# Performance work log

Hardware: AMD Instinct MI355X
Metric: run time of the kernel (lower is better)

Reference implementation:

```python
import jax, jax.numpy as jnp
import numpy as np

N = 8192       # num_nodes
E = 262144     # num_edges (avg degree 32)
D_IN = 256
D_H = 256
D_OUT = 256
BN_EPS = 1e-5


def _linear_params(key, din, dout):
    # torch nn.Linear default init: U(-1/sqrt(din), 1/sqrt(din))
    s = 1.0 / np.sqrt(din)
    kw, kb = jax.random.split(key)
    W = jax.random.uniform(kw, (dout, din), jnp.float32, -s, s)
    b = jax.random.uniform(kb, (dout,), jnp.float32, -s, s)
    return W, b


def setup_inputs() -> dict:
    key = jax.random.key(0)
    ks = jax.random.split(key, 6)
    x = jax.random.normal(ks[0], (N, D_IN), jnp.float32)
    edge_index = jax.random.randint(ks[1], (2, E), 0, N, dtype=jnp.int64)
    W1, b1 = _linear_params(ks[2], D_IN, D_H)
    W2, b2 = _linear_params(ks[3], D_H, D_H)
    W3, b3 = _linear_params(ks[4], D_H, D_OUT)
    return {
        "x": x, "edge_index": edge_index,
        "W1": W1, "b1": b1, "W2": W2, "b2": b2, "W3": W3, "b3": b3,
        "g1": jnp.ones((D_H,), jnp.float32), "be1": jnp.zeros((D_H,), jnp.float32),
        "g2": jnp.ones((D_H,), jnp.float32), "be2": jnp.zeros((D_H,), jnp.float32),
        "g3": jnp.ones((D_OUT,), jnp.float32), "be3": jnp.zeros((D_OUT,), jnp.float32),
    }


def _build_norm(edge_index):
    # add self loops, scatter 1.0 into dense NxN adjacency (duplicates collapse via set)
    loop = jnp.arange(N, dtype=edge_index.dtype)
    rows = jnp.concatenate([edge_index[0], loop])
    cols = jnp.concatenate([edge_index[1], loop])
    adj = jnp.zeros((N, N), jnp.float32).at[rows, cols].set(1.0)
    deg = adj.sum(axis=1)
    dinv = jnp.where(deg > 0, deg ** -0.5, 0.0)  # inf -> 0 as in original
    return dinv[:, None] * adj * dinv[None, :]


def _gcn(x, norm, W, b):
    # linear then symmetric-normalized aggregation
    return norm @ (x @ W.T + b)


def _bn(x, g, b):
    # BatchNorm1d with batch statistics (biased var), eps=1e-5
    mu = x.mean(axis=0)
    var = x.var(axis=0)
    return (x - mu) * jax.lax.rsqrt(var + BN_EPS) * g + b


def reference(x, edge_index, W1, b1, W2, b2, W3, b3, g1, be1, g2, be2, g3, be3):
    norm = _build_norm(edge_index)
    h = jax.nn.relu(_bn(_gcn(x, norm, W1, b1), g1, be1))
    h = jax.nn.relu(_bn(_gcn(h, norm, W2, b2), g2, be2))
    h = _bn(_gcn(h, norm, W3, b3), g3, be3)
    return h
```

## Files before the change

kernel.cpp:

```cpp
#include <hip/hip_runtime.h>

#define N_NODES 8192
#define N_EDGES 262144
#define D 256
#define ADJ_WORDS 256
#define MAX_DEG 128
#define AGG_BLOCKS 2048
#define RED_BLOCKS 128

typedef __attribute__((ext_vector_type(8))) short bf16x8;
typedef __attribute__((ext_vector_type(4))) float f32x4;

__device__ __forceinline__ short f2bf(float f) {
    unsigned u = __builtin_bit_cast(unsigned, f);
    u += 0x7fffu + ((u >> 16) & 1);
    return (short)(u >> 16);
}
__device__ __forceinline__ float bf2f(unsigned short u) {
    return __builtin_bit_cast(float, ((unsigned)u) << 16);
}

__global__ void build_adj(const int* __restrict__ ei, unsigned* __restrict__ adj,
                          int* __restrict__ deg) {
    int i = blockIdx.x * blockDim.x + threadIdx.x;
    int r, c;
    if (i < N_EDGES) {
        r = ei[i];
        c = ei[N_EDGES + i];
    } else if (i < N_EDGES + N_NODES) {
        r = i - N_EDGES;
        c = r;
    } else {
        return;
    }
    unsigned bit = 1u << (c & 31);
    unsigned old = atomicOr(&adj[r * ADJ_WORDS + (c >> 5)], bit);
    if (!(old & bit)) atomicAdd(&deg[r], 1);
}

__global__ __launch_bounds__(256) void build_nbrs(const unsigned* __restrict__ adj,
                                                  const int* __restrict__ deg,
                                                  int* __restrict__ nbr_idx,
                                                  float* __restrict__ nbr_w,
                                                  const float* __restrict__ W1,
                                                  const float* __restrict__ W2,
                                                  const float* __restrict__ W3,
                                                  unsigned short* __restrict__ Wb1,
                                                  unsigned short* __restrict__ Wb2,
                                                  unsigned short* __restrict__ Wb3) {
    if (blockIdx.x >= N_NODES) {
        int i = (blockIdx.x - N_NODES) * 256 + threadIdx.x;
        int which = i >> 16, j = i & 65535;
        const float* src = which == 0 ? W1 : which == 1 ? W2 : W3;
        unsigned short* dst = which == 0 ? Wb1 : which == 1 ? Wb2 : Wb3;
        dst[j] = (unsigned short)f2bf(src[j]);
        return;
    }
    const int r = blockIdx.x;
    const int t = threadIdx.x;
    const int lane = t & 63, wave = t >> 6;
    unsigned m = adj[r * ADJ_WORDS + t];
    int cnt = __popc(m);
    int x = cnt;
    #pragma unroll
    for (int off = 1; off < 64; off <<= 1) {
        int v = __shfl_up(x, off, 64);
        if (lane >= off) x += v;
    }
    __shared__ int wtot[4];
    if (lane == 63) wtot[wave] = x;
    __syncthreads();
    int woff = 0;
    #pragma unroll
    for (int w = 0; w < 4; w++) woff += (w < wave) ? wtot[w] : 0;
    int base = woff + x - cnt;
    const float dr = rsqrtf((float)deg[r]);
    int* oi = nbr_idx + (size_t)r * MAX_DEG;
    float* ow = nbr_w + (size_t)r * MAX_DEG;
    while (m) {
        int b = __ffs(m) - 1;
        m &= m - 1;
        int c = (t << 5) + b;
        if (base < MAX_DEG) {
            oi[base] = c;
            ow[base] = dr * rsqrtf((float)deg[c]);
        }
        base++;
    }
}

template <bool APPLY, bool RELU>
__global__ __launch_bounds__(256) void gemm_mfma(const float* __restrict__ Xsrc,
                                                 const float* __restrict__ psum2,
                                                 const float* __restrict__ psq2,
                                                 const float* __restrict__ g,
                                                 const float* __restrict__ be,
                                                 const unsigned short* __restrict__ Wb,
                                                 const float* __restrict__ bias,
                                                 unsigned short* __restrict__ Hb) {
    __shared__ float ssc[256], ssh[256];
    const int tid = threadIdx.x;
    if (APPLY) {
        float s = 0.f, q = 0.f;
        #pragma unroll 8
        for (int i = 0; i < RED_BLOCKS; i++) {
            s += psum2[i * 256 + tid];
            q += psq2[i * 256 + tid];
        }
        float mu = s * (1.0f / N_NODES);
        float var = q * (1.0f / N_NODES) - mu * mu;
        float rstd = rsqrtf(var + 1e-5f);
        float sc = g[tid] * rstd;
        ssc[tid] = sc;
        ssh[tid] = be[tid] - mu * sc;
        __syncthreads();
    }

    const int bn = blockIdx.x * 64;
    const int bm = blockIdx.y * 128;
    const int wave = tid >> 6, lane = tid & 63;
    const int l16 = lane & 15, q = lane >> 4;
    const int mrow0 = bm + wave * 32;

    f32x4 acc[2][4];
    #pragma unroll
    for (int i = 0; i < 2; i++)
        #pragma unroll
        for (int j = 0; j < 4; j++) acc[i][j] = (f32x4){0.f, 0.f, 0.f, 0.f};

    for (int k0 = 0; k0 < D; k0 += 32) {
        const int kq = k0 + q * 8;
        bf16x8 xb[2];
        float4 sc0, sc1, sh0, sh1;
        if (APPLY) {
            sc0 = *(const float4*)(ssc + kq);
            sc1 = *(const float4*)(ssc + kq + 4);
            sh0 = *(const float4*)(ssh + kq);
            sh1 = *(const float4*)(ssh + kq + 4);
        }
        #pragma unroll
        for (int mf = 0; mf < 2; mf++) {
            const float* xr = Xsrc + (size_t)(mrow0 + mf * 16 + l16) * D + kq;
            float4 a = *(const float4*)xr;
            float4 b = *(const float4*)(xr + 4);
            float v[8] = {a.x, a.y, a.z, a.w, b.x, b.y, b.z, b.w};
            if (APPLY) {
                float sc[8] = {sc0.x, sc0.y, sc0.z, sc0.w, sc1.x, sc1.y, sc1.z, sc1.w};
                float sh[8] = {sh0.x, sh0.y, sh0.z, sh0.w, sh1.x, sh1.y, sh1.z, sh1.w};
                #pragma unroll
                for (int j = 0; j < 8; j++) {
                    v[j] = fmaf(v[j], sc[j], sh[j]);
                    if (RELU) v[j] = fmaxf(v[j], 0.0f);
                }
            }
            #pragma unroll
            for (int j = 0; j < 8; j++) xb[mf][j] = f2bf(v[j]);
        }
        #pragma unroll
        for (int nf = 0; nf < 4; nf++) {
            bf16x8 wa = *(const bf16x8*)(Wb + (size_t)(bn + nf * 16 + l16) * D + kq);
            #pragma unroll
            for (int mf = 0; mf < 2; mf++)
                acc[mf][nf] = __builtin_amdgcn_mfma_f32_16x16x32_bf16(wa, xb[mf], acc[mf][nf], 0, 0, 0);
        }
    }

    #pragma unroll
    for (int mf = 0; mf < 2; mf++) {
        const int m = mrow0 + mf * 16 + l16;
        #pragma unroll
        for (int nf = 0; nf < 4; nf++) {
            const int nb = bn + nf * 16 + q * 4;
            float4 b4 = *(const float4*)(bias + nb);
            short4 o;
            o.x = f2bf(acc[mf][nf][0] + b4.x);
            o.y = f2bf(acc[mf][nf][1] + b4.y);
            o.z = f2bf(acc[mf][nf][2] + b4.z);
            o.w = f2bf(acc[mf][nf][3] + b4.w);
            *(short4*)(Hb + (size_t)m * D + nb) = o;
        }
    }
}

__global__ __launch_bounds__(256) void aggregate_bf16(const int* __restrict__ nbr_idx,
                                                      const float* __restrict__ nbr_w,
                                                      const int* __restrict__ deg,
                                                      const unsigned short* __restrict__ Hb,
                                                      float* __restrict__ G,
                                                      float* __restrict__ psum,
                                                      float* __restrict__ psumsq) {
    const int wave = threadIdx.x >> 6;
    const int lane = threadIdx.x & 63;
    const int ch = lane * 4;
    const int r = blockIdx.x * 4 + wave;

    int dg = deg[r]; if (dg > MAX_DEG) dg = MAX_DEG;
    const int* idx = nbr_idx + (size_t)r * MAX_DEG;
    const float* wt = nbr_w + (size_t)r * MAX_DEG;
    float4 A = make_float4(0.f, 0.f, 0.f, 0.f);
    int j = 0;
    for (; j + 8 <= dg; j += 8) {
        int4 c0 = *(const int4*)(idx + j);
        int4 c1 = *(const int4*)(idx + j + 4);
        float4 w0 = *(const float4*)(wt + j);
        float4 w1 = *(const float4*)(wt + j + 4);
        ushort4 u0 = *(const ushort4*)(Hb + (size_t)c0.x * D + ch);
        ushort4 u1 = *(const ushort4*)(Hb + (size_t)c0.y * D + ch);
        ushort4 u2 = *(const ushort4*)(Hb + (size_t)c0.z * D + ch);
        ushort4 u3 = *(const ushort4*)(Hb + (size_t)c0.w * D + ch);
        ushort4 u4 = *(const ushort4*)(Hb + (size_t)c1.x * D + ch);
        ushort4 u5 = *(const ushort4*)(Hb + (size_t)c1.y * D + ch);
        ushort4 u6 = *(const ushort4*)(Hb + (size_t)c1.z * D + ch);
        ushort4 u7 = *(const ushort4*)(Hb + (size_t)c1.w * D + ch);
        A.x = fmaf(w0.x, bf2f(u0.x), A.x); A.y = fmaf(w0.x, bf2f(u0.y), A.y);
        A.z = fmaf(w0.x, bf2f(u0.z), A.z); A.w = fmaf(w0.x, bf2f(u0.w), A.w);
        A.x = fmaf(w0.y, bf2f(u1.x), A.x); A.y = fmaf(w0.y, bf2f(u1.y), A.y);
        A.z = fmaf(w0.y, bf2f(u1.z), A.z); A.w = fmaf(w0.y, bf2f(u1.w), A.w);
        A.x = fmaf(w0.z, bf2f(u2.x), A.x); A.y = fmaf(w0.z, bf2f(u2.y), A.y);
        A.z = fmaf(w0.z, bf2f(u2.z), A.z); A.w = fmaf(w0.z, bf2f(u2.w), A.w);
        A.x = fmaf(w0.w, bf2f(u3.x), A.x); A.y = fmaf(w0.w, bf2f(u3.y), A.y);
        A.z = fmaf(w0.w, bf2f(u3.z), A.z); A.w = fmaf(w0.w, bf2f(u3.w), A.w);
        A.x = fmaf(w1.x, bf2f(u4.x), A.x); A.y = fmaf(w1.x, bf2f(u4.y), A.y);
        A.z = fmaf(w1.x, bf2f(u4.z), A.z); A.w = fmaf(w1.x, bf2f(u4.w), A.w);
        A.x = fmaf(w1.y, bf2f(u5.x), A.x); A.y = fmaf(w1.y, bf2f(u5.y), A.y);
        A.z = fmaf(w1.y, bf2f(u5.z), A.z); A.w = fmaf(w1.y, bf2f(u5.w), A.w);
        A.x = fmaf(w1.z, bf2f(u6.x), A.x); A.y = fmaf(w1.z, bf2f(u6.y), A.y);
        A.z = fmaf(w1.z, bf2f(u6.z), A.z); A.w = fmaf(w1.z, bf2f(u6.w), A.w);
        A.x = fmaf(w1.w, bf2f(u7.x), A.x); A.y = fmaf(w1.w, bf2f(u7.y), A.y);
        A.z = fmaf(w1.w, bf2f(u7.z), A.z); A.w = fmaf(w1.w, bf2f(u7.w), A.w);
    }
    for (; j + 4 <= dg; j += 4) {
        int4 c0 = *(const int4*)(idx + j);
        float4 w0 = *(const float4*)(wt + j);
        ushort4 u0 = *(const ushort4*)(Hb + (size_t)c0.x * D + ch);
        ushort4 u1 = *(const ushort4*)(Hb + (size_t)c0.y * D + ch);
        ushort4 u2 = *(const ushort4*)(Hb + (size_t)c0.z * D + ch);
        ushort4 u3 = *(const ushort4*)(Hb + (size_t)c0.w * D + ch);
        A.x = fmaf(w0.x, bf2f(u0.x), A.x); A.y = fmaf(w0.x, bf2f(u0.y), A.y);
        A.z = fmaf(w0.x, bf2f(u0.z), A.z); A.w = fmaf(w0.x, bf2f(u0.w), A.w);
        A.x = fmaf(w0.y, bf2f(u1.x), A.x); A.y = fmaf(w0.y, bf2f(u1.y), A.y);
        A.z = fmaf(w0.y, bf2f(u1.z), A.z); A.w = fmaf(w0.y, bf2f(u1.w), A.w);
        A.x = fmaf(w0.z, bf2f(u2.x), A.x); A.y = fmaf(w0.z, bf2f(u2.y), A.y);
        A.z = fmaf(w0.z, bf2f(u2.z), A.z); A.w = fmaf(w0.z, bf2f(u2.w), A.w);
        A.x = fmaf(w0.w, bf2f(u3.x), A.x); A.y = fmaf(w0.w, bf2f(u3.y), A.y);
        A.z = fmaf(w0.w, bf2f(u3.z), A.z); A.w = fmaf(w0.w, bf2f(u3.w), A.w);
    }
    for (; j < dg; j++) {
        int c = idx[j];
        float w = wt[j];
        ushort4 u = *(const ushort4*)(Hb + (size_t)c * D + ch);
        A.x = fmaf(w, bf2f(u.x), A.x); A.y = fmaf(w, bf2f(u.y), A.y);
        A.z = fmaf(w, bf2f(u.z), A.z); A.w = fmaf(w, bf2f(u.w), A.w);
    }
    *(float4*)(G + (size_t)r * D + ch) = A;

    __shared__ float ls[4][256], lss[4][256];
    ls[wave][ch] = A.x; ls[wave][ch + 1] = A.y; ls[wave][ch + 2] = A.z; ls[wave][ch + 3] = A.w;
    lss[wave][ch] = A.x * A.x; lss[wave][ch + 1] = A.y * A.y;
    lss[wave][ch + 2] = A.z * A.z; lss[wave][ch + 3] = A.w * A.w;
    __syncthreads();
    const int t = threadIdx.x;
    psum[blockIdx.x * 256 + t] = ls[0][t] + ls[1][t] + ls[2][t] + ls[3][t];
    psumsq[blockIdx.x * 256 + t] = lss[0][t] + lss[1][t] + lss[2][t] + lss[3][t];
}

__global__ __launch_bounds__(256) void reduce_partials(const float* __restrict__ psum,
                                                       const float* __restrict__ psumsq,
                                                       float* __restrict__ psum2,
                                                       float* __restrict__ psumsq2) {
    const int b = blockIdx.x;
    const int t = threadIdx.x;
    const int rows = AGG_BLOCKS / RED_BLOCKS;
    float s = 0.0f, q = 0.0f;
    #pragma unroll
    for (int i = 0; i < rows; i++) {
        s += psum[(size_t)(b * rows + i) * 256 + t];
        q += psumsq[(size_t)(b * rows + i) * 256 + t];
    }
    psum2[b * 256 + t] = s;
    psumsq2[b * 256 + t] = q;
}

__global__ __launch_bounds__(256) void bn_apply_out(const float* __restrict__ G,
                                                    const float* __restrict__ psum2,
                                                    const float* __restrict__ psq2,
                                                    const float* __restrict__ g,
                                                    const float* __restrict__ be,
                                                    float* __restrict__ Out) {
    __shared__ float ssc[256], ssh[256];
    const int tid = threadIdx.x;
    {
        float s = 0.f, q = 0.f;
        #pragma unroll 8
        for (int i = 0; i < RED_BLOCKS; i++) {
            s += psum2[i * 256 + tid];
            q += psq2[i * 256 + tid];
        }
        float mu = s * (1.0f / N_NODES);
        float var = q * (1.0f / N_NODES) - mu * mu;
        float rstd = rsqrtf(var + 1e-5f);
        float sc = g[tid] * rstd;
        ssc[tid] = sc;
        ssh[tid] = be[tid] - mu * sc;
        __syncthreads();
    }
    const int rows_per_block = 64;
    const int r0 = blockIdx.x * rows_per_block;
    const int ch = (tid & 63) * 4;
    const int rsub = tid >> 6;
    float4 sc = *(const float4*)(ssc + ch);
    float4 sh = *(const float4*)(ssh + ch);
    for (int rr = rsub; rr < rows_per_block; rr += 4) {
        const size_t off = (size_t)(r0 + rr) * D + ch;
        float4 v = *(const float4*)(G + off);
        v.x = fmaf(v.x, sc.x, sh.x);
        v.y = fmaf(v.y, sc.y, sh.y);
        v.z = fmaf(v.z, sc.z, sh.z);
        v.w = fmaf(v.w, sc.w, sh.w);
        *(float4*)(Out + off) = v;
    }
}

extern "C" void kernel_launch(void* const* d_in, const int* in_sizes, int n_in,
                              void* d_out, int out_size, void* d_ws, size_t ws_size,
                              hipStream_t stream) {
    const float* x  = (const float*)d_in[0];
    const int*   ei = (const int*)d_in[1];
    const float* W1 = (const float*)d_in[2];
    const float* b1 = (const float*)d_in[3];
    const float* W2 = (const float*)d_in[4];
    const float* b2 = (const float*)d_in[5];
    const float* W3 = (const float*)d_in[6];
    const float* b3 = (const float*)d_in[7];
    const float* g1 = (const float*)d_in[8];
    const float* be1 = (const float*)d_in[9];
    const float* g2 = (const float*)d_in[10];
    const float* be2 = (const float*)d_in[11];
    const float* g3 = (const float*)d_in[12];
    const float* be3 = (const float*)d_in[13];

    char* ws = (char*)d_ws;
    unsigned*       adj  = (unsigned*)ws;
    unsigned short* Hb   = (unsigned short*)ws;
    int*            deg  = (int*)(ws + (8 << 20));
    float*          psum2= (float*)(ws + (8 << 20) + (64 << 10));
    float*          psq2 = (float*)(ws + (8 << 20) + (192 << 10));
    unsigned short* Wb1  = (unsigned short*)(ws + (8 << 20) + (320 << 10));
    unsigned short* Wb2  = (unsigned short*)(ws + (8 << 20) + (448 << 10));
    unsigned short* Wb3  = (unsigned short*)(ws + (8 << 20) + (576 << 10));
    float*          psum = (float*)(ws + (9 << 20));
    float*          psq  = (float*)(ws + (11 << 20));
    int*            nbr_idx = (int*)  (ws + (13 << 20));
    float*          nbr_w   = (float*)(ws + (17 << 20));
    float*          G       = (float*)(ws + (21 << 20));

    hipMemsetAsync(ws, 0, (8 << 20) + (32 << 10), stream);

    build_adj<<<(N_EDGES + N_NODES + 255) / 256, 256, 0, stream>>>(ei, adj, deg);
    build_nbrs<<<N_NODES + 768, 256, 0, stream>>>(adj, deg, nbr_idx, nbr_w,
                                                  W1, W2, W3, Wb1, Wb2, Wb3);

    dim3 ggrid(D / 64, N_NODES / 128);

    gemm_mfma<false, false><<<ggrid, 256, 0, stream>>>(x, nullptr, nullptr, nullptr, nullptr,
                                                       Wb1, b1, Hb);
    aggregate_bf16<<<AGG_BLOCKS, 256, 0, stream>>>(nbr_idx, nbr_w, deg, Hb, G, psum, psq);
    reduce_partials<<<RED_BLOCKS, 256, 0, stream>>>(psum, psq, psum2, psq2);

    gemm_mfma<true, true><<<ggrid, 256, 0, stream>>>(G, psum2, psq2, g1, be1, Wb2, b2, Hb);
    aggregate_bf16<<<AGG_BLOCKS, 256, 0, stream>>>(nbr_idx, nbr_w, deg, Hb, G, psum, psq);
    reduce_partials<<<RED_BLOCKS, 256, 0, stream>>>(psum, psq, psum2, psq2);

    gemm_mfma<true, true><<<ggrid, 256, 0, stream>>>(G, psum2, psq2, g2, be2, Wb3, b3, Hb);
    aggregate_bf16<<<AGG_BLOCKS, 256, 0, stream>>>(nbr_idx, nbr_w, deg, Hb, G, psum, psq);
    reduce_partials<<<RED_BLOCKS, 256, 0, stream>>>(psum, psq, psum2, psq2);

    bn_apply_out<<<N_NODES / 64, 256, 0, stream>>>(G, psum2, psq2, g3, be3, (float*)d_out);
}
```

Baseline: 237.3 us.

## Store intermediate aggregates as bf16, shrink GEMM tile, unroll gather by 16

The first two layers' aggregation outputs are now written as bf16 instead of fp32. The following GEMM reads them as bf16, which halves the intermediate traffic between the aggregate and GEMM kernels. The GEMM M-tile is halved to 64 rows per block with one 16-row fragment per wave, doubling the block count. The aggregation gather loop is unrolled to 16 neighbours to keep more loads in flight. The bf16 rounding happens before batch-norm, which adds quantization error, and each block now reuses fewer weights.

New measurement: 251.9 us. 1.06x slower.

```diff
diff --git a/kernel.cpp b/kernel.cpp
--- a/kernel.cpp
+++ b/kernel.cpp
@@ -89,8 +89,8 @@
     }
 }
 
-template <bool APPLY, bool RELU>
-__global__ __launch_bounds__(256) void gemm_mfma(const float* __restrict__ Xsrc,
+template <bool APPLY, bool RELU, bool XBF16>
+__global__ __launch_bounds__(256) void gemm_mfma(const void* __restrict__ Xsrc,
                                                  const float* __restrict__ psum2,
                                                  const float* __restrict__ psq2,
                                                  const float* __restrict__ g,
@@ -117,75 +117,72 @@
     }
 
     const int bn = blockIdx.x * 64;
-    const int bm = blockIdx.y * 128;
+    const int bm = blockIdx.y * 64;
     const int wave = tid >> 6, lane = tid & 63;
     const int l16 = lane & 15, q = lane >> 4;
-    const int mrow0 = bm + wave * 32;
-
-    f32x4 acc[2][4];
+    const int mrow = bm + wave * 16 + l16;
+
+    f32x4 acc[4];
     #pragma unroll
-    for (int i = 0; i < 2; i++)
-        #pragma unroll
-        for (int j = 0; j < 4; j++) acc[i][j] = (f32x4){0.f, 0.f, 0.f, 0.f};
+    for (int j = 0; j < 4; j++) acc[j] = (f32x4){0.f, 0.f, 0.f, 0.f};
 
     for (int k0 = 0; k0 < D; k0 += 32) {
         const int kq = k0 + q * 8;
-        bf16x8 xb[2];
-        float4 sc0, sc1, sh0, sh1;
-        if (APPLY) {
-            sc0 = *(const float4*)(ssc + kq);
-            sc1 = *(const float4*)(ssc + kq + 4);
-            sh0 = *(const float4*)(ssh + kq);
-            sh1 = *(const float4*)(ssh + kq + 4);
-        }
-        #pragma unroll
-        for (int mf = 0; mf < 2; mf++) {
-            const float* xr = Xsrc + (size_t)(mrow0 + mf * 16 + l16) * D + kq;
+        bf16x8 xb;
+        float v[8];
+        if (XBF16) {
+            bf16x8 xr = *(const bf16x8*)((const unsigned short*)Xsrc + (size_t)mrow * D + kq);
+            #pragma unroll
+            for (int j = 0; j < 8; j++) v[j] = bf2f((unsigned short)xr[j]);
+        } else {
+            const float* xr = (const float*)Xsrc + (size_t)mrow * D + kq;
             float4 a = *(const float4*)xr;
             float4 b = *(const float4*)(xr + 4);
-            float v[8] = {a.x, a.y, a.z, a.w, b.x, b.y, b.z, b.w};
-            if (APPLY) {
-                float sc[8] = {sc0.x, sc0.y, sc0.z, sc0.w, sc1.x, sc1.y, sc1.z, sc1.w};
-                float sh[8] = {sh0.x, sh0.y, sh0.z, sh0.w, sh1.x, sh1.y, sh1.z, sh1.w};
-                #pragma unroll
-                for (int j = 0; j < 8; j++) {
-                    v[j] = fmaf(v[j], sc[j], sh[j]);
-                    if (RELU) v[j] = fmaxf(v[j], 0.0f);
-                }
+            v[0] = a.x; v[1] = a.y; v[2] = a.z; v[3] = a.w;
+            v[4] = b.x; v[5] = b.y; v[6] = b.z; v[7] = b.w;
+        }
+        if (APPLY) {
+            float4 sc0 = *(const float4*)(ssc + kq);
+            float4 sc1 = *(const float4*)(ssc + kq + 4);
+            float4 sh0 = *(const float4*)(ssh + kq);
+            float4 sh1 = *(const float4*)(ssh + kq + 4);
+            float sc[8] = {sc0.x, sc0.y, sc0.z, sc0.w, sc1.x, sc1.y, sc1.z, sc1.w};
+            float sh[8] = {sh0.x, sh0.y, sh0.z, sh0.w, sh1.x, sh1.y, sh1.z, sh1.w};
+            #pragma unroll
+            for (int j = 0; j < 8; j++) {
+                v[j] = fmaf(v[j], sc[j], sh[j]);
+                if (RELU) v[j] = fmaxf(v[j], 0.0f);
             }
-            #pragma unroll
-            for (int j = 0; j < 8; j++) xb[mf][j] = f2bf(v[j]);
-        }
+        }
+        #pragma unroll
+        for (int j = 0; j < 8; j++) xb[j] = f2bf(v[j]);
+
         #pragma unroll
         for (int nf = 0; nf < 4; nf++) {
             bf16x8 wa = *(const bf16x8*)(Wb + (size_t)(bn + nf * 16 + l16) * D + kq);
-            #pragma unroll
-            for (int mf = 0; mf < 2; mf++)
-                acc[mf][nf] = __builtin_amdgcn_mfma_f32_16x16x32_bf16(wa, xb[mf], acc[mf][nf], 0, 0, 0);
+            acc[nf] = __builtin_amdgcn_mfma_f32_16x16x32_bf16(wa, xb, acc[nf], 0, 0, 0);
         }
     }
 
     #pragma unroll
-    for (int mf = 0; mf < 2; mf++) {
-        const int m = mrow0 + mf * 16 + l16;
-        #pragma unroll
-        for (int nf = 0; nf < 4; nf++) {
-            const int nb = bn + nf * 16 + q * 4;
-            float4 b4 = *(const float4*)(bias + nb);
-            short4 o;
-            o.x = f2bf(acc[mf][nf][0] + b4.x);
-            o.y = f2bf(acc[mf][nf][1] + b4.y);
-            o.z = f2bf(acc[mf][nf][2] + b4.z);
-            o.w = f2bf(acc[mf][nf][3] + b4.w);
-            *(short4*)(Hb + (size_t)m * D + nb) = o;
-        }
-    }
-}
-
+    for (int nf = 0; nf < 4; nf++) {
+        const int nb = bn + nf * 16 + q * 4;
+        float4 b4 = *(const float4*)(bias + nb);
+        short4 o;
+        o.x = f2bf(acc[nf][0] + b4.x);
+        o.y = f2bf(acc[nf][1] + b4.y);
+        o.z = f2bf(acc[nf][2] + b4.z);
+        o.w = f2bf(acc[nf][3] + b4.w);
+        *(short4*)(Hb + (size_t)mrow * D + nb) = o;
+    }
+}
+
+template <bool LAST>
 __global__ __launch_bounds__(256) void aggregate_bf16(const int* __restrict__ nbr_idx,
                                                       const float* __restrict__ nbr_w,
                                                       const int* __restrict__ deg,
                                                       const unsigned short* __restrict__ Hb,
+                                                      unsigned short* __restrict__ Gb,
                                                       float* __restrict__ G,
                                                       float* __restrict__ psum,
                                                       float* __restrict__ psumsq) {
@@ -199,11 +196,15 @@
     const float* wt = nbr_w + (size_t)r * MAX_DEG;
     float4 A = make_float4(0.f, 0.f, 0.f, 0.f);
     int j = 0;
-    for (; j + 8 <= dg; j += 8) {
+    for (; j + 16 <= dg; j += 16) {
         int4 c0 = *(const int4*)(idx + j);
         int4 c1 = *(const int4*)(idx + j + 4);
+        int4 c2 = *(const int4*)(idx + j + 8);
+        int4 c3 = *(const int4*)(idx + j + 12);
         float4 w0 = *(const float4*)(wt + j);
         float4 w1 = *(const float4*)(wt + j + 4);
+        float4 w2 = *(const float4*)(wt + j + 8);
+        float4 w3 = *(const float4*)(wt + j + 12);
         ushort4 u0 = *(const ushort4*)(Hb + (size_t)c0.x * D + ch);
         ushort4 u1 = *(const ushort4*)(Hb + (size_t)c0.y * D + ch);
         ushort4 u2 = *(const ushort4*)(Hb + (size_t)c0.z * D + ch);
@@ -212,6 +213,14 @@
         ushort4 u5 = *(const ushort4*)(Hb + (size_t)c1.y * D + ch);
         ushort4 u6 = *(const ushort4*)(Hb + (size_t)c1.z * D + ch);
         ushort4 u7 = *(const ushort4*)(Hb + (size_t)c1.w * D + ch);
+        ushort4 u8 = *(const ushort4*)(Hb + (size_t)c2.x * D + ch);
+        ushort4 u9 = *(const ushort4*)(Hb + (size_t)c2.y * D + ch);
+        ushort4 ua = *(const ushort4*)(Hb + (size_t)c2.z * D + ch);
+        ushort4 ub = *(const ushort4*)(Hb + (size_t)c2.w * D + ch);
+        ushort4 uc = *(const ushort4*)(Hb + (size_t)c3.x * D + ch);
+        ushort4 ud = *(const ushort4*)(Hb + (size_t)c3.y * D + ch);
+        ushort4 ue = *(const ushort4*)(Hb + (size_t)c3.z * D + ch);
+        ushort4 uf = *(const ushort4*)(Hb + (size_t)c3.w * D + ch);
         A.x = fmaf(w0.x, bf2f(u0.x), A.x); A.y = fmaf(w0.x, bf2f(u0.y), A.y);
         A.z = fmaf(w0.x, bf2f(u0.z), A.z); A.w = fmaf(w0.x, bf2f(u0.w), A.w);
         A.x = fmaf(w0.y, bf2f(u1.x), A.x); A.y = fmaf(w0.y, bf2f(u1.y), A.y);
@@ -228,6 +237,22 @@
         A.z = fmaf(w1.z, bf2f(u6.z), A.z); A.w = fmaf(w1.z, bf2f(u6.w), A.w);
         A.x = fmaf(w1.w, bf2f(u7.x), A.x); A.y = fmaf(w1.w, bf2f(u7.y), A.y);
         A.z = fmaf(w1.w, bf2f(u7.z), A.z); A.w = fmaf(w1.w, bf2f(u7.w), A.w);
+        A.x = fmaf(w2.x, bf2f(u8.x), A.x); A.y = fmaf(w2.x, bf2f(u8.y), A.y);
+        A.z = fmaf(w2.x, bf2f(u8.z), A.z); A.w = fmaf(w2.x, bf2f(u8.w), A.w);
+        A.x = fmaf(w2.y, bf2f(u9.x), A.x); A.y = fmaf(w2.y, bf2f(u9.y), A.y);
+        A.z = fmaf(w2.y, bf2f(u9.z), A.z); A.w = fmaf(w2.y, bf2f(u9.w), A.w);
+        A.x = fmaf(w2.z, bf2f(ua.x), A.x); A.y = fmaf(w2.z, bf2f(ua.y), A.y);
+        A.z = fmaf(w2.z, bf2f(ua.z), A.z); A.w = fmaf(w2.z, bf2f(ua.w), A.w);
+        A.x = fmaf(w2.w, bf2f(ub.x), A.x); A.y = fmaf(w2.w, bf2f(ub.y), A.y);
+        A.z = fmaf(w2.w, bf2f(ub.z), A.z); A.w = fmaf(w2.w, bf2f(ub.w), A.w);
+        A.x = fmaf(w3.x, bf2f(uc.x), A.x); A.y = fmaf(w3.x, bf2f(uc.y), A.y);
+        A.z = fmaf(w3.x, bf2f(uc.z), A.z); A.w = fmaf(w3.x, bf2f(uc.w), A.w);
+        A.x = fmaf(w3.y, bf2f(ud.x), A.x); A.y = fmaf(w3.y, bf2f(ud.y), A.y);
+        A.z = fmaf(w3.y, bf2f(ud.z), A.z); A.w = fmaf(w3.y, bf2f(ud.w), A.w);
+        A.x = fmaf(w3.z, bf2f(ue.x), A.x); A.y = fmaf(w3.z, bf2f(ue.y), A.y);
+        A.z = fmaf(w3.z, bf2f(ue.z), A.z); A.w = fmaf(w3.z, bf2f(ue.w), A.w);
+        A.x = fmaf(w3.w, bf2f(uf.x), A.x); A.y = fmaf(w3.w, bf2f(uf.y), A.y);
+        A.z = fmaf(w3.w, bf2f(uf.z), A.z); A.w = fmaf(w3.w, bf2f(uf.w), A.w);
     }
     for (; j + 4 <= dg; j += 4) {
         int4 c0 = *(const int4*)(idx + j);
@@ -252,7 +277,12 @@
         A.x = fmaf(w, bf2f(u.x), A.x); A.y = fmaf(w, bf2f(u.y), A.y);
         A.z = fmaf(w, bf2f(u.z), A.z); A.w = fmaf(w, bf2f(u.w), A.w);
     }
-    *(float4*)(G + (size_t)r * D + ch) = A;
+    if (LAST) {
+        *(float4*)(G + (size_t)r * D + ch) = A;
+    } else {
+        short4 o = {f2bf(A.x), f2bf(A.y), f2bf(A.z), f2bf(A.w)};
+        *(short4*)(Gb + (size_t)r * D + ch) = o;
+    }
 
     __shared__ float ls[4][256], lss[4][256];
     ls[wave][ch] = A.x; ls[wave][ch + 1] = A.y; ls[wave][ch + 2] = A.z; ls[wave][ch + 3] = A.w;
@@ -353,6 +383,7 @@
     int*            nbr_idx = (int*)  (ws + (13 << 20));
     float*          nbr_w   = (float*)(ws + (17 << 20));
     float*          G       = (float*)(ws + (21 << 20));
+    unsigned short* Gb      = (unsigned short*)(ws + (21 << 20));
 
     hipMemsetAsync(ws, 0, (8 << 20) + (32 << 10), stream);
 
@@ -360,19 +391,22 @@
     build_nbrs<<<N_NODES + 768, 256, 0, stream>>>(adj, deg, nbr_idx, nbr_w,
                                                   W1, W2, W3, Wb1, Wb2, Wb3);
 
-    dim3 ggrid(D / 64, N_NODES / 128);
-
-    gemm_mfma<false, false><<<ggrid, 256, 0, stream>>>(x, nullptr, nullptr, nullptr, nullptr,
-                                                       Wb1, b1, Hb);
-    aggregate_bf16<<<AGG_BLOCKS, 256, 0, stream>>>(nbr_idx, nbr_w, deg, Hb, G, psum, psq);
+    dim3 ggrid(D / 64, N_NODES / 64);
+
+    gemm_mfma<false, false, false><<<ggrid, 256, 0, stream>>>(x, nullptr, nullptr, nullptr,
+                                                              nullptr, Wb1, b1, Hb);
+    aggregate_bf16<false><<<AGG_BLOCKS, 256, 0, stream>>>(nbr_idx, nbr_w, deg, Hb, Gb, nullptr,
+                                                          psum, psq);
     reduce_partials<<<RED_BLOCKS, 256, 0, stream>>>(psum, psq, psum2, psq2);
 
-    gemm_mfma<true, true><<<ggrid, 256, 0, stream>>>(G, psum2, psq2, g1, be1, Wb2, b2, Hb);
-    aggregate_bf16<<<AGG_BLOCKS, 256, 0, stream>>>(nbr_idx, nbr_w, deg, Hb, G, psum, psq);
+    gemm_mfma<true, true, true><<<ggrid, 256, 0, stream>>>(Gb, psum2, psq2, g1, be1, Wb2, b2, Hb);
+    aggregate_bf16<false><<<AGG_BLOCKS, 256, 0, stream>>>(nbr_idx, nbr_w, deg, Hb, Gb, nullptr,
+                                                          psum, psq);
     reduce_partials<<<RED_BLOCKS, 256, 0, stream>>>(psum, psq, psum2, psq2);
 
-    gemm_mfma<true, true><<<ggrid, 256, 0, stream>>>(G, psum2, psq2, g2, be2, Wb3, b3, Hb);
-    aggregate_bf16<<<AGG_BLOCKS, 256, 0, stream>>>(nbr_idx, nbr_w, deg, Hb, G, psum, psq);
+    gemm_mfma<true, true, true><<<ggrid, 256, 0, stream>>>(Gb, psum2, psq2, g2, be2, Wb3, b3, Hb);
+    aggregate_bf16<true><<<AGG_BLOCKS, 256, 0, stream>>>(nbr_idx, nbr_w, deg, Hb, nullptr, G,
+                                                         psum, psq);
     reduce_partials<<<RED_BLOCKS, 256, 0, stream>>>(psum, psq, psum2, psq2);
 
     bn_apply_out<<<N_NODES / 64, 256, 0, stream>>>(G, psum2, psq2, g3, be3, (float*)d_out);
```
